# Optimization experiments

Hardware: AMD Instinct MI355X
Metric: run time of the kernel (lower is better)

Reference implementation:

```python
import jax, jax.numpy as jnp
import numpy as np

NUM_GROUPS = 32
NUM_HEAD_CH = 64
EPS = 1e-5


def setup_inputs() -> dict:
    key = jax.random.key(0)
    k1, k2, k3 = jax.random.split(key, 3)
    B, C, H, W = 16, 512, 32, 32
    return {
        "x": jax.random.normal(k1, (B, C, H, W), dtype=jnp.float32),
        "norm_w": jnp.ones((C,), dtype=jnp.float32),
        "norm_b": jnp.zeros((C,), dtype=jnp.float32),
        "qkv_w": jax.random.normal(k2, (3 * C, C), dtype=jnp.float32) * 0.02,
        "qkv_b": jnp.zeros((3 * C,), dtype=jnp.float32),
        "proj_w": jax.random.normal(k3, (C, C), dtype=jnp.float32) * 0.02,
        "proj_b": jnp.zeros((C,), dtype=jnp.float32),
    }


def _group_norm(x, w, b):
    # x: [B, C, T]
    B, C, T = x.shape
    g = x.reshape(B, NUM_GROUPS, C // NUM_GROUPS, T)
    mean = g.mean(axis=(2, 3), keepdims=True)
    var = g.var(axis=(2, 3), keepdims=True)
    g = (g - mean) * jax.lax.rsqrt(var + EPS)
    return g.reshape(B, C, T) * w[None, :, None] + b[None, :, None]


def reference(x, norm_w, norm_b, qkv_w, qkv_b, proj_w, proj_b):
    B, C, Hs, Ws = x.shape
    T = Hs * Ws
    xr = x.reshape(B, C, T)
    xn = _group_norm(xr, norm_w, norm_b)
    # 1x1 conv == matmul over channel dim
    qkv = jnp.einsum('oc,bct->bot', qkv_w, xn) + qkv_b[None, :, None]  # [B, 3C, T]
    q, k, v = jnp.split(qkv, 3, axis=1)
    nH = C // NUM_HEAD_CH
    ch = NUM_HEAD_CH
    q = q.reshape(B * nH, ch, T)
    k = k.reshape(B * nH, ch, T)
    v = v.reshape(B * nH, ch, T)
    scale = 1.0 / np.sqrt(np.sqrt(ch)).astype(np.float32)
    # [BH, T, S] score matrix, softmax in float32 (matches torch .float())
    weight = jnp.einsum('bct,bcs->bts', q * scale, k * scale)
    weight = jax.nn.softmax(weight.astype(jnp.float32), axis=-1).astype(weight.dtype)
    a = jnp.einsum('bts,bcs->bct', weight, v).reshape(B, C, T)
    h = jnp.einsum('oc,bct->bot', proj_w, a) + proj_b[None, :, None]
    return (xr + h).reshape(B, C, Hs, Ws)
```

## Files before the change

kernel.cpp:

```cpp
#include <hip/hip_runtime.h>
#include <hip/hip_bf16.h>


typedef __bf16 bf16x8 __attribute__((ext_vector_type(8)));
typedef __bf16 bf16x4 __attribute__((ext_vector_type(4)));
typedef float f32x4 __attribute__((ext_vector_type(4)));

#define MFMA16(a, b, c) __builtin_amdgcn_mfma_f32_16x16x32_bf16((a), (b), (c), 0, 0, 0)

typedef const __attribute__((address_space(1))) unsigned int* gptr_t;
typedef __attribute__((address_space(3))) unsigned int* lptr_t;

__device__ __forceinline__ void gload16(const void* g, void* l) {
  __builtin_amdgcn_global_load_lds((gptr_t)g, (lptr_t)l, 16, 0, 0);
}

__global__ __launch_bounds__(256) void gn_cvt_kernel(const float* __restrict__ x,
                                                     const float* __restrict__ nw,
                                                     const float* __restrict__ nb,
                                                     __hip_bfloat16* __restrict__ xnt,
                                                     const float* __restrict__ qw,
                                                     __hip_bfloat16* __restrict__ qwb,
                                                     const float* __restrict__ pw,
                                                     __hip_bfloat16* __restrict__ pwb) {
  const int blk = blockIdx.x;
  if (blk >= 512) {
    const int base = (blk - 512) * 256 + threadIdx.x;
#pragma unroll
    for (int t = 0; t < 4; ++t) {
      int i = base + t * 65536;
      const float* src;
      __hip_bfloat16* dst;
      if (i < 196608) { src = qw; dst = qwb; }
      else            { i -= 196608; src = pw; dst = pwb; }
      float4 v = ((const float4*)src)[i];
      union { __hip_bfloat16 h[4]; uint2 u; } pk;
      pk.h[0] = __float2bfloat16(v.x);
      pk.h[1] = __float2bfloat16(v.y);
      pk.h[2] = __float2bfloat16(v.z);
      pk.h[3] = __float2bfloat16(v.w);
      *(uint2*)(dst + (size_t)i * 4) = pk.u;
    }
    return;
  }
  const int bb = blk & 15, g = blk >> 4;
  const int tid = threadIdx.x;
  const float4* xg = (const float4*)(x + ((size_t)bb * 512 + g * 16) * 1024);

  float4 vals[16];
  float s = 0.f, ss = 0.f;
#pragma unroll
  for (int k = 0; k < 16; ++k) {
    float4 v = xg[tid + 256 * k];
    vals[k] = v;
    s += v.x + v.y + v.z + v.w;
    ss += v.x * v.x + v.y * v.y + v.z * v.z + v.w * v.w;
  }
#pragma unroll
  for (int off = 1; off < 64; off <<= 1) {
    s += __shfl_xor(s, off, 64);
    ss += __shfl_xor(ss, off, 64);
  }
  __shared__ float red[8];
  const int wid = tid >> 6, lane = tid & 63;
  if (lane == 0) { red[wid] = s; red[wid + 4] = ss; }
  __syncthreads();
  s = red[0] + red[1] + red[2] + red[3];
  ss = red[4] + red[5] + red[6] + red[7];
  const float mean = s * (1.f / 16384.f);
  const float var = ss * (1.f / 16384.f) - mean * mean;
  const float rstd = rsqrtf(var + 1e-5f);

  float aa[16], cc[16];
#pragma unroll
  for (int k = 0; k < 16; ++k) {
    float w = nw[g * 16 + k];
    float b = nb[g * 16 + k];
    aa[k] = rstd * w;
    cc[k] = b - mean * aa[k];
  }
#pragma unroll
  for (int j = 0; j < 4; ++j) {
    union { __hip_bfloat16 h[16]; uint4 u[2]; } row;
#pragma unroll
    for (int k = 0; k < 16; ++k) {
      float v = ((const float*)&vals[k])[j];
      row.h[k] = __float2bfloat16(v * aa[k] + cc[k]);
    }
    size_t idx = ((size_t)bb * 1024 + 4 * tid + j) * 512 + g * 16;
    *(uint4*)(xnt + idx) = row.u[0];
    *(uint4*)(xnt + idx + 8) = row.u[1];
  }
}

template <int EPI>
__global__ __launch_bounds__(512) void gemm_bt(const __hip_bfloat16* __restrict__ A,
                                               const __hip_bfloat16* __restrict__ Bt,
                                               const float* __restrict__ bias,
                                               __hip_bfloat16* __restrict__ oq,
                                               __hip_bfloat16* __restrict__ ok,
                                               __hip_bfloat16* __restrict__ ov,
                                               const float* __restrict__ xres,
                                               float* __restrict__ of) {
  __shared__ __hip_bfloat16 Alds[128 * 64];
  __shared__ __hip_bfloat16 Blds[256 * 64];
  const int tid = threadIdx.x;
  const int wid = tid >> 6, lane = tid & 63;
  const int g = lane >> 4, tl = lane & 15;
  const int wr = wid >> 2, wc = wid & 3;
  const int NM = (EPI == 0) ? 12 : 4;
  const int id = blockIdx.x;
  const int xcd = id & 7, w = id >> 3;
  const int m0 = (w % NM) * 128;
  const int n0 = (xcd * 8 + w / NM) * 256;

  const int srow8 = lane >> 3;
  const int sselem = ((lane & 7) * 8) ^ (srow8 << 3);
  const int rswz = (tl & 7) << 4;

  f32x4 acc[4][4];
#pragma unroll
  for (int i = 0; i < 4; ++i)
#pragma unroll
    for (int j = 0; j < 4; ++j) acc[i][j] = (f32x4){0.f, 0.f, 0.f, 0.f};

  for (int kt = 0; kt < 8; ++kt) {
    const int k0 = kt * 64;
    __syncthreads();
#pragma unroll
    for (int q = 0; q < 2; ++q) {
      const int r = q * 64 + wid * 8 + srow8;
      gload16(A + (size_t)(m0 + r) * 512 + k0 + sselem,
              (char*)Alds + q * 8192 + wid * 1024);
    }
#pragma unroll
    for (int q = 0; q < 4; ++q) {
      const int r = q * 64 + wid * 8 + srow8;
      gload16(Bt + (size_t)(n0 + r) * 512 + k0 + sselem,
              (char*)Blds + q * 8192 + wid * 1024);
    }
    __syncthreads();
#pragma unroll
    for (int kk = 0; kk < 2; ++kk) {
      bf16x8 af[4], bfr[4];
#pragma unroll
      for (int mi = 0; mi < 4; ++mi) {
        const int row = wr * 64 + mi * 16 + tl;
        af[mi] = *(const bf16x8*)((char*)Alds + row * 128 + ((kk * 64 + g * 16) ^ rswz));
      }
#pragma unroll
      for (int ni = 0; ni < 4; ++ni) {
        const int row = wc * 64 + ni * 16 + tl;
        bfr[ni] = *(const bf16x8*)((char*)Blds + row * 128 + ((kk * 64 + g * 16) ^ rswz));
      }
      __builtin_amdgcn_s_setprio(1);
#pragma unroll
      for (int mi = 0; mi < 4; ++mi)
#pragma unroll
        for (int ni = 0; ni < 4; ++ni)
          acc[mi][ni] = MFMA16(af[mi], bfr[ni], acc[mi][ni]);
      __builtin_amdgcn_s_setprio(0);
    }
  }

  if (EPI == 0) {
    const bool isv = (m0 >= 1024);
    const bool isq = (m0 < 512);
    const float qs = 0.42466090014286f;
#pragma unroll
    for (int mi = 0; mi < 4; ++mi) {
      const int o = m0 + wr * 64 + mi * 16 + g * 4;
      const int och = o & 511, h = och >> 6, cb = och & 63;
#pragma unroll
      for (int ni = 0; ni < 4; ++ni) {
        const int n = n0 + wc * 64 + ni * 16 + tl;
        const int bb2 = n >> 10, t = n & 1023;
        const int bh = bb2 * 8 + h;
        if (!isv) {
          union { __hip_bfloat16 h4[4]; uint2 u; } pk;
#pragma unroll
          for (int r = 0; r < 4; ++r)
            pk.h4[r] = __float2bfloat16((acc[mi][ni][r] + bias[o + r]) * qs);
          __hip_bfloat16* dst = (isq ? oq : ok) + ((size_t)bh * 1024 + t) * 64 + cb;
          *(uint2*)dst = pk.u;
        } else {
#pragma unroll
          for (int r = 0; r < 4; ++r)
            ov[((size_t)bh * 64 + cb + r) * 1024 + t] =
                __float2bfloat16(acc[mi][ni][r] + bias[o + r]);
        }
      }
    }
  } else {
#pragma unroll
    for (int mi = 0; mi < 4; ++mi) {
#pragma unroll
      for (int r = 0; r < 4; ++r) {
        const int o = m0 + wr * 64 + mi * 16 + g * 4 + r;
        const float bv = bias[o];
#pragma unroll
        for (int ni = 0; ni < 4; ++ni) {
          const int n = n0 + wc * 64 + ni * 16 + tl;
          const int bb2 = n >> 10, t = n & 1023;
          const size_t xi = ((size_t)bb2 * 512 + o) * 1024 + t;
          of[xi] = xres[xi] + acc[mi][ni][r] + bv;
        }
      }
    }
  }
}

__global__ __launch_bounds__(512) void attn_kernel(
    const __hip_bfloat16* __restrict__ qt,
    const __hip_bfloat16* __restrict__ kt,
    const __hip_bfloat16* __restrict__ vv,
    __hip_bfloat16* __restrict__ at) {
  const int blk = blockIdx.x;
  const int xcd = blk & 7;
  const int within = blk >> 3;
  const int tile = within & 3;
  const int bhi = xcd * 16 + (within >> 2);
  const int tid = threadIdx.x;
  const int wid = tid >> 6, lane = tid & 63;
  const int g = lane >> 4, tl = lane & 15;
  const int t0 = tile * 256 + wid * 32;

  const char* qh = (const char*)(qt + (size_t)bhi * 65536);
  const char* kh = (const char*)(kt + (size_t)bhi * 65536);
  const char* vh = (const char*)(vv + (size_t)bhi * 65536);

  __shared__ __hip_bfloat16 Klds[3][4096];
  __shared__ __hip_bfloat16 Vlds[3][4096];
  __shared__ __hip_bfloat16 Plds[8][2048];

  const int swz = (tl & 7) << 4;
  char* Pw = (char*)&Plds[wid][0];

  const int srow = lane >> 3;
  const int grow = wid * 8 + srow;
  const int ssw = ((lane & 7) * 16) ^ ((srow & 7) << 4);

  bf16x8 qb[2][2];
#pragma unroll
  for (int qs = 0; qs < 2; ++qs)
#pragma unroll
    for (int h = 0; h < 2; ++h)
      qb[qs][h] = *(const bf16x8*)(qh + (size_t)(t0 + qs * 16 + tl) * 128 + h * 64 + g * 16);

  bf16x8 vones;
#pragma unroll
  for (int i = 0; i < 8; ++i) vones[i] = (__bf16)1.0f;

  f32x4 acc[2][4];
  f32x4 accl[2];
#pragma unroll
  for (int i = 0; i < 2; ++i) {
    accl[i] = (f32x4){0.f, 0.f, 0.f, 0.f};
#pragma unroll
    for (int j = 0; j < 4; ++j) acc[i][j] = (f32x4){0.f, 0.f, 0.f, 0.f};
  }

  gload16(kh + (size_t)grow * 128 + ssw, (char*)&Klds[0][0] + wid * 1024);
  gload16(vh + (size_t)grow * 2048 + ssw, (char*)&Vlds[0][0] + wid * 1024);
  gload16(kh + (size_t)(64 + grow) * 128 + ssw, (char*)&Klds[1][0] + wid * 1024);
  gload16(vh + (size_t)grow * 2048 + 128 + ssw, (char*)&Vlds[1][0] + wid * 1024);
  asm volatile("s_waitcnt vmcnt(2)" ::: "memory");
  __builtin_amdgcn_s_barrier();

  for (int sb = 0; sb < 16; ++sb) {
    {
      const int nt = (sb + 2) & 15;
      const int nbuf = (sb + 2) % 3;
      gload16(kh + (size_t)(nt * 64 + grow) * 128 + ssw,
              (char*)&Klds[nbuf][0] + wid * 1024);
      gload16(vh + (size_t)grow * 2048 + nt * 128 + ssw,
              (char*)&Vlds[nbuf][0] + wid * 1024);
    }
    const int cb = sb % 3;
    const char* Kb = (const char*)&Klds[cb][0];
    const char* Vb = (const char*)&Vlds[cb][0];

    f32x4 sv[4][2];
#pragma unroll
    for (int st = 0; st < 4; ++st) {
      const int krow = (st * 16 + tl) * 128;
      bf16x8 ka0 = *(const bf16x8*)(Kb + krow + ((g * 16) ^ swz));
      bf16x8 ka1 = *(const bf16x8*)(Kb + krow + ((64 + g * 16) ^ swz));
      __builtin_amdgcn_s_setprio(1);
#pragma unroll
      for (int qs = 0; qs < 2; ++qs) {
        f32x4 z = (f32x4){0.f, 0.f, 0.f, 0.f};
        z = MFMA16(ka0, qb[qs][0], z);
        z = MFMA16(ka1, qb[qs][1], z);
        sv[st][qs] = z;
      }
      __builtin_amdgcn_s_setprio(0);
    }

#pragma unroll
    for (int qs = 0; qs < 2; ++qs) {
#pragma unroll
      for (int st = 0; st < 4; ++st) {
        bf16x4 pu;
#pragma unroll
        for (int r = 0; r < 4; ++r) {
          float p = exp2f(sv[st][qs][r]);
          pu[r] = (__bf16)p;
        }
        *(bf16x4*)(Pw + (qs * 16 + tl) * 128 + ((st * 32 + g * 8) ^ swz)) = pu;
      }
    }

    bf16x8 pa[2][2];
#pragma unroll
    for (int ts = 0; ts < 2; ++ts) {
      const int prow = (ts * 16 + tl) * 128;
      pa[ts][0] = *(const bf16x8*)(Pw + prow + ((g * 16) ^ swz));
      pa[ts][1] = *(const bf16x8*)(Pw + prow + ((64 + g * 16) ^ swz));
    }
    __builtin_amdgcn_s_setprio(1);
#pragma unroll
    for (int ts = 0; ts < 2; ++ts) {
      accl[ts] = MFMA16(pa[ts][0], vones, accl[ts]);
      accl[ts] = MFMA16(pa[ts][1], vones, accl[ts]);
    }
    __builtin_amdgcn_s_setprio(0);
#pragma unroll
    for (int ct = 0; ct < 4; ++ct) {
      const int vrow = (ct * 16 + tl) * 128;
      bf16x8 vb0 = *(const bf16x8*)(Vb + vrow + ((g * 16) ^ swz));
      bf16x8 vb1 = *(const bf16x8*)(Vb + vrow + ((64 + g * 16) ^ swz));
      __builtin_amdgcn_s_setprio(1);
#pragma unroll
      for (int ts = 0; ts < 2; ++ts) {
        acc[ts][ct] = MFMA16(pa[ts][0], vb0, acc[ts][ct]);
        acc[ts][ct] = MFMA16(pa[ts][1], vb1, acc[ts][ct]);
      }
      __builtin_amdgcn_s_setprio(0);
    }
    asm volatile("s_waitcnt vmcnt(2)" ::: "memory");
    __builtin_amdgcn_s_barrier();
  }

  const int bb2 = bhi >> 3, hh = bhi & 7;
#pragma unroll
  for (int ts = 0; ts < 2; ++ts) {
#pragma unroll
    for (int r = 0; r < 4; ++r) {
      const float iv = 1.f / accl[ts][r];
      const size_t row = (size_t)bb2 * 1024 + t0 + ts * 16 + g * 4 + r;
#pragma unroll
      for (int ct = 0; ct < 4; ++ct)
        at[row * 512 + hh * 64 + ct * 16 + tl] = __float2bfloat16(acc[ts][ct][r] * iv);
    }
  }
}

extern "C" void kernel_launch(void* const* d_in, const int* in_sizes, int n_in,
                              void* d_out, int out_size, void* d_ws, size_t ws_size,
                              hipStream_t stream) {
  const float* x  = (const float*)d_in[0];
  const float* nw = (const float*)d_in[1];
  const float* nb = (const float*)d_in[2];
  const float* qw = (const float*)d_in[3];
  const float* qb = (const float*)d_in[4];
  const float* pw = (const float*)d_in[5];
  const float* pb = (const float*)d_in[6];
  float* out = (float*)d_out;
  char* ws = (char*)d_ws;

  __hip_bfloat16* xnt = (__hip_bfloat16*)(ws);
  __hip_bfloat16* qtb = (__hip_bfloat16*)(ws + 16777216);
  __hip_bfloat16* ktb = (__hip_bfloat16*)(ws + 33554432);
  __hip_bfloat16* vvb = (__hip_bfloat16*)(ws + 50331648);
  __hip_bfloat16* qwb = (__hip_bfloat16*)(ws + 67108864);
  __hip_bfloat16* pwb = (__hip_bfloat16*)(ws + 68681728);

  gn_cvt_kernel<<<768, 256, 0, stream>>>(x, nw, nb, xnt, qw, qwb, pw, pwb);
  gemm_bt<0><<<768, 512, 0, stream>>>(qwb, xnt, qb, qtb, ktb, vvb,
                                      nullptr, nullptr);
  attn_kernel<<<512, 512, 0, stream>>>(qtb, ktb, vvb, xnt);
  gemm_bt<1><<<256, 512, 0, stream>>>(pwb, xnt, pb, nullptr, nullptr,
                                      nullptr, x, out);
}
```

Before: 136.3 us.

## Shrink attention blocks to 4 waves with double-buffered K/V tiles

The attention kernel now launches 1024 blocks of 256 threads, each covering 128 query rows instead of 256. The K/V pipeline goes from a three-stage ring with partial vmcnt waits to a two-buffer ping-pong with full __syncthreads. Each wave now loads 16 rows instead of 8. The intent is to cut LDS per block so more blocks fit per CU and there are more blocks to spread across CUs. The cost is that each K/V tile is loaded twice as many times in total, and the full wait at every step exposes more memory latency.

```diff
diff --git a/kernel.cpp b/kernel.cpp
--- a/kernel.cpp
+++ b/kernel.cpp
@@ -210,7 +210,7 @@
   }
 }
 
-__global__ __launch_bounds__(512) void attn_kernel(
+__global__ __launch_bounds__(256) void attn_kernel(
     const __hip_bfloat16* __restrict__ qt,
     const __hip_bfloat16* __restrict__ kt,
     const __hip_bfloat16* __restrict__ vv,
@@ -218,26 +218,26 @@
   const int blk = blockIdx.x;
   const int xcd = blk & 7;
   const int within = blk >> 3;
-  const int tile = within & 3;
-  const int bhi = xcd * 16 + (within >> 2);
+  const int tile = within & 7;
+  const int bhi = xcd * 16 + (within >> 3);
   const int tid = threadIdx.x;
   const int wid = tid >> 6, lane = tid & 63;
   const int g = lane >> 4, tl = lane & 15;
-  const int t0 = tile * 256 + wid * 32;
+  const int t0 = tile * 128 + wid * 32;
 
   const char* qh = (const char*)(qt + (size_t)bhi * 65536);
   const char* kh = (const char*)(kt + (size_t)bhi * 65536);
   const char* vh = (const char*)(vv + (size_t)bhi * 65536);
 
-  __shared__ __hip_bfloat16 Klds[3][4096];
-  __shared__ __hip_bfloat16 Vlds[3][4096];
-  __shared__ __hip_bfloat16 Plds[8][2048];
+  __shared__ __hip_bfloat16 Klds[2][4096];
+  __shared__ __hip_bfloat16 Vlds[2][4096];
+  __shared__ __hip_bfloat16 Plds[4][2048];
 
   const int swz = (tl & 7) << 4;
   char* Pw = (char*)&Plds[wid][0];
 
   const int srow = lane >> 3;
-  const int grow = wid * 8 + srow;
+  const int rb0 = wid * 16;
   const int ssw = ((lane & 7) * 16) ^ ((srow & 7) << 4);
 
   bf16x8 qb[2][2];
@@ -260,25 +260,31 @@
     for (int j = 0; j < 4; ++j) acc[i][j] = (f32x4){0.f, 0.f, 0.f, 0.f};
   }
 
-  gload16(kh + (size_t)grow * 128 + ssw, (char*)&Klds[0][0] + wid * 1024);
-  gload16(vh + (size_t)grow * 2048 + ssw, (char*)&Vlds[0][0] + wid * 1024);
-  gload16(kh + (size_t)(64 + grow) * 128 + ssw, (char*)&Klds[1][0] + wid * 1024);
-  gload16(vh + (size_t)grow * 2048 + 128 + ssw, (char*)&Vlds[1][0] + wid * 1024);
-  asm volatile("s_waitcnt vmcnt(2)" ::: "memory");
-  __builtin_amdgcn_s_barrier();
-
+#pragma unroll
+  for (int q2 = 0; q2 < 2; ++q2) {
+    const int r = rb0 + q2 * 8 + srow;
+    gload16(kh + (size_t)r * 128 + ssw,
+            (char*)&Klds[0][0] + (rb0 + q2 * 8) * 128);
+    gload16(vh + (size_t)r * 2048 + ssw,
+            (char*)&Vlds[0][0] + (rb0 + q2 * 8) * 128);
+  }
+  __syncthreads();
+
+  int cur = 0;
   for (int sb = 0; sb < 16; ++sb) {
-    {
-      const int nt = (sb + 2) & 15;
-      const int nbuf = (sb + 2) % 3;
-      gload16(kh + (size_t)(nt * 64 + grow) * 128 + ssw,
-              (char*)&Klds[nbuf][0] + wid * 1024);
-      gload16(vh + (size_t)grow * 2048 + nt * 128 + ssw,
-              (char*)&Vlds[nbuf][0] + wid * 1024);
-    }
-    const int cb = sb % 3;
-    const char* Kb = (const char*)&Klds[cb][0];
-    const char* Vb = (const char*)&Vlds[cb][0];
+    if (sb < 15) {
+      const int s0n = (sb + 1) * 64;
+#pragma unroll
+      for (int q2 = 0; q2 < 2; ++q2) {
+        const int r = rb0 + q2 * 8 + srow;
+        gload16(kh + (size_t)(s0n + r) * 128 + ssw,
+                (char*)&Klds[cur ^ 1][0] + (rb0 + q2 * 8) * 128);
+        gload16(vh + (size_t)r * 2048 + s0n * 2 + ssw,
+                (char*)&Vlds[cur ^ 1][0] + (rb0 + q2 * 8) * 128);
+      }
+    }
+    const char* Kb = (const char*)&Klds[cur][0];
+    const char* Vb = (const char*)&Vlds[cur][0];
 
     f32x4 sv[4][2];
 #pragma unroll
@@ -338,8 +344,8 @@
       }
       __builtin_amdgcn_s_setprio(0);
     }
-    asm volatile("s_waitcnt vmcnt(2)" ::: "memory");
-    __builtin_amdgcn_s_barrier();
+    __syncthreads();
+    cur ^= 1;
   }
 
   const int bb2 = bhi >> 3, hh = bhi & 7;
@@ -379,7 +385,7 @@
   gn_cvt_kernel<<<768, 256, 0, stream>>>(x, nw, nb, xnt, qw, qwb, pw, pwb);
   gemm_bt<0><<<768, 512, 0, stream>>>(qwb, xnt, qb, qtb, ktb, vvb,
                                       nullptr, nullptr);
-  attn_kernel<<<512, 512, 0, stream>>>(qtb, ktb, vvb, xnt);
+  attn_kernel<<<1024, 256, 0, stream>>>(qtb, ktb, vvb, xnt);
   gemm_bt<1><<<256, 512, 0, stream>>>(pwb, xnt, pb, nullptr, nullptr,
                                       nullptr, x, out);
 }
```

Measured after the change: 148.8 us. 1.09x slower.
